# Performance work log

Hardware: AMD Instinct MI355X
Metric: run time of the kernel (lower is better)

Reference implementation:

```python
import jax, jax.numpy as jnp
import numpy as np

# E2M1 FP4 value table: codes 0-7 positive, 8-15 negative (sign bit = MSB)
FP4_LUT = jnp.array([0.0, 0.5, 1.0, 1.5, 2.0, 3.0, 4.0, 6.0,
                     -0.0, -0.5, -1.0, -1.5, -2.0, -3.0, -4.0, -6.0],
                    dtype=jnp.float32)
GROUP = 32  # MX microscaling block size


def _dequant(codes, scales):
    # codes: [O, I] int in [0,16); scales: [O, I//GROUP] power-of-two floats
    vals = FP4_LUT[codes]                          # [O, I]
    return vals * jnp.repeat(scales, GROUP, axis=1)  # broadcast group scale


def setup_inputs() -> dict:
    key = jax.random.key(0)
    ks = jax.random.split(key, 7)
    T, D, G = 8192, 4096, GROUP
    x = jax.random.normal(ks[0], (T, D), dtype=jnp.float32)
    w1_codes = jax.random.randint(ks[1], (D, D), 0, 16, dtype=jnp.int32)
    w1_scales = (2.0 ** jax.random.randint(ks[2], (D, D // G), -6, 2)).astype(jnp.float32)
    b1 = jax.random.normal(ks[3], (D,), dtype=jnp.float32) * 0.01
    w2_codes = jax.random.randint(ks[4], (D, D), 0, 16, dtype=jnp.int32)
    w2_scales = (2.0 ** jax.random.randint(ks[5], (D, D // G), -6, 2)).astype(jnp.float32)
    b2 = jax.random.normal(ks[6], (D,), dtype=jnp.float32) * 0.01
    return {"x": x, "w1_codes": w1_codes, "w1_scales": w1_scales, "b1": b1,
            "w2_codes": w2_codes, "w2_scales": w2_scales, "b2": b2}


def reference(x, w1_codes, w1_scales, b1, w2_codes, w2_scales, b2):
    # first MXFP4 quant linear: y = x @ dequant(W1)^T + b1
    h = x @ _dequant(w1_codes, w1_scales).T + b1
    # second MXFP4 quant linear
    y = h @ _dequant(w2_codes, w2_scales).T + b2
    return y
```

## Files before the change

### kernel.cpp

```cpp
#include <hip/hip_runtime.h>


typedef __bf16 bf16;
typedef bf16 bf16x8 __attribute__((ext_vector_type(8)));
typedef float f32x4 __attribute__((ext_vector_type(4)));
typedef int intx4 __attribute__((ext_vector_type(4)));

#define T_DIM 8192
#define D_DIM 4096

__device__ __forceinline__ void gld_lds16(const void* g, void* l) {
    __builtin_amdgcn_global_load_lds(
        (const __attribute__((address_space(1))) void*)g,
        (__attribute__((address_space(3))) void*)l,
        16, 0, 0);
}

__global__ __launch_bounds__(256) void dequant_kernel(
    const int* __restrict__ codes, const float* __restrict__ scales,
    bf16* __restrict__ out)
{
    const size_t tid = (size_t)blockIdx.x * 256 + threadIdx.x;
    const size_t e = tid * 8;
    const int row = (int)(e >> 12);
    const int col = (int)(e & 4095);
    const float s = scales[(size_t)row * (D_DIM / 32) + (col >> 5)];
    const intx4 c0 = *(const intx4*)(codes + e);
    const intx4 c1 = *(const intx4*)(codes + e + 4);
    bf16x8 o;
#pragma unroll
    for (int i = 0; i < 8; ++i) {
        const int c = (i < 4) ? c0[i] : c1[i - 4];
        float v = (float)((0xC8643210u >> ((c & 7) * 4)) & 0xF) * 0.5f;
        v = (c & 8) ? -v : v;
        o[i] = (bf16)(v * s);
    }
    *(bf16x8*)(out + e) = o;
}

__global__ __launch_bounds__(256) void f32_to_bf16_kernel(
    const float* __restrict__ in, bf16* __restrict__ out)
{
    const size_t tid = (size_t)blockIdx.x * 256 + threadIdx.x;
    const size_t e = tid * 8;
    const float4 a = *(const float4*)(in + e);
    const float4 b = *(const float4*)(in + e + 4);
    bf16x8 o;
    o[0] = (bf16)a.x; o[1] = (bf16)a.y; o[2] = (bf16)a.z; o[3] = (bf16)a.w;
    o[4] = (bf16)b.x; o[5] = (bf16)b.y; o[6] = (bf16)b.z; o[7] = (bf16)b.w;
    *(bf16x8*)(out + e) = o;
}

__device__ __forceinline__ bf16x8 fragr(const char* slot, int row, int qbs) {
    return *(const bf16x8*)(slot + row * 64 + qbs);
}

template <bool OUT_BF16>
__global__ __launch_bounds__(512, 2) void gemm_bt_8ph(
    const bf16* __restrict__ A, const bf16* __restrict__ B,
    const float* __restrict__ bias, void* __restrict__ Cout,
    int M, int N, int K)
{
    __shared__ alignas(128) char lds[131072];
    char* ldsA = lds;
    char* ldsB = lds + 65536;

    const int u = threadIdx.x;
    const int lane = u & 63;
    const int wave = u >> 6;
    const int wm = wave >> 2;
    const int wn = wave & 3;
    const int fr = lane & 15;
    const int qbs = ((lane >> 4) * 16) ^ ((fr & 6) << 3);

    const int nwg = gridDim.x * gridDim.y;
    const int bid0 = blockIdx.y * gridDim.x + blockIdx.x;
    const int cpx = nwg >> 3;
    const int sbid = (bid0 & 7) * cpx + (bid0 >> 3);
    const int m0 = (sbid / gridDim.x) * 256;
    const int n0 = (sbid % gridDim.x) * 256;

    const int r0 = u >> 2;
    const int cb = ((u & 3) * 16) ^ ((r0 & 6) << 3);
    const bf16* pa = A + (size_t)(m0 + r0) * K + (cb >> 1);
    const bf16* pb = B + (size_t)(n0 + r0) * K + (cb >> 1);
    const size_t rstep = (size_t)128 * K;

#define STAGE_A(SLOT, KB) do {                                                 \
    gld_lds16(pa + (KB),         ldsA + (SLOT) * 16384 + u * 16);              \
    gld_lds16(pa + rstep + (KB), ldsA + (SLOT) * 16384 + 8192 + u * 16);       \
  } while (0)
#define STAGE_B(SLOT, KB) do {                                                 \
    gld_lds16(pb + (KB),         ldsB + (SLOT) * 16384 + u * 16);              \
    gld_lds16(pb + rstep + (KB), ldsB + (SLOT) * 16384 + 8192 + u * 16);       \
  } while (0)
#define AS(s) (ldsA + (s) * 16384)
#define BS(s) (ldsB + (s) * 16384)

    const int arow0 = wm * 128 + fr;
    const int brow0 = wn * 64 + fr;

    f32x4 acc[8][4] = {};
    bf16x8 aq[4], bq[4];

#define PHASE(ASLOT, BSLOT, MH, READB, STAGE_STMT, DO_VM)                      \
  do {                                                                         \
    if (READB) {                                                               \
      bq[0] = fragr(BSLOT, brow0,      qbs);                                   \
      bq[1] = fragr(BSLOT, brow0 + 16, qbs);                                   \
      bq[2] = fragr(BSLOT, brow0 + 32, qbs);                                   \
      bq[3] = fragr(BSLOT, brow0 + 48, qbs);                                   \
    }                                                                          \
    aq[0] = fragr(ASLOT, arow0 + (MH) * 64,      qbs);                         \
    aq[1] = fragr(ASLOT, arow0 + (MH) * 64 + 16, qbs);                         \
    aq[2] = fragr(ASLOT, arow0 + (MH) * 64 + 32, qbs);                         \
    aq[3] = fragr(ASLOT, arow0 + (MH) * 64 + 48, qbs);                         \
    STAGE_STMT;                                                                \
    __builtin_amdgcn_s_barrier();                                              \
    asm volatile("s_waitcnt lgkmcnt(0)" ::: "memory");                         \
    __builtin_amdgcn_s_setprio(1);                                             \
    _Pragma("unroll")                                                          \
    for (int jj = 0; jj < 4; ++jj) {                                           \
      _Pragma("unroll")                                                        \
      for (int ii = 0; ii < 4; ++ii)                                           \
        acc[(MH) * 4 + ii][jj] = __builtin_amdgcn_mfma_f32_16x16x32_bf16(      \
            aq[ii], bq[jj], acc[(MH) * 4 + ii][jj], 0, 0, 0);                  \
    }                                                                          \
    __builtin_amdgcn_s_setprio(0);                                             \
    if (DO_VM) { asm volatile("s_waitcnt vmcnt(6)" ::: "memory"); }            \
    __builtin_amdgcn_s_barrier();                                              \
  } while (0)

    STAGE_A(0, 0);
    STAGE_B(0, 0);
    STAGE_A(1, 32);
    STAGE_B(1, 32);
    STAGE_A(2, 64);
    STAGE_B(2, 64);
    STAGE_B(3, 96);
    asm volatile("s_waitcnt vmcnt(6)" ::: "memory");
    __builtin_amdgcn_s_barrier();

    const int NT = K >> 6;
    const int NI = NT >> 1;

    for (int it = 0; it < NI; ++it) {
        const int t = it * 2;
        const int k1 = (t + 1) * 64;
        const int k2 = ((t + 2) < NT ? (t + 2) : (NT - 1)) * 64;
        const int k3 = ((t + 3) < NT ? (t + 3) : (NT - 1)) * 64;
        PHASE(AS(0), BS(0), 0, 1, STAGE_A(3, k1 + 32), 0);
        PHASE(AS(0), BS(0), 1, 0, STAGE_B(0, k2),      0);
        PHASE(AS(1), BS(1), 0, 1, STAGE_A(0, k2),      0);
        PHASE(AS(1), BS(1), 1, 0, STAGE_B(1, k2 + 32), 1);
        PHASE(AS(2), BS(2), 0, 1, STAGE_A(1, k2 + 32), 0);
        PHASE(AS(2), BS(2), 1, 0, STAGE_B(2, k3),      0);
        PHASE(AS(3), BS(3), 0, 1, STAGE_A(2, k3),      0);
        PHASE(AS(3), BS(3), 1, 0, STAGE_B(3, k3 + 32), 1);
    }

#undef PHASE
#undef STAGE_A
#undef STAGE_B
#undef AS
#undef BS

    const int cn = fr;
    const int q4 = (lane >> 4) * 4;
#pragma unroll
    for (int j = 0; j < 4; ++j) {
        const int gn = n0 + wn * 64 + j * 16 + cn;
        const float bv = bias[gn];
#pragma unroll
        for (int mf = 0; mf < 8; ++mf) {
            const int gm = m0 + wm * 128 + mf * 16 + q4;
#pragma unroll
            for (int r = 0; r < 4; ++r) {
                const float v = acc[mf][j][r] + bv;
                const size_t idx = (size_t)(gm + r) * N + gn;
                if (OUT_BF16) ((bf16*)Cout)[idx] = (bf16)v;
                else          ((float*)Cout)[idx] = v;
            }
        }
    }
    (void)M;
}

extern "C" void kernel_launch(void* const* d_in, const int* in_sizes, int n_in,
                              void* d_out, int out_size, void* d_ws, size_t ws_size,
                              hipStream_t stream)
{
    const float* x         = (const float*)d_in[0];
    const int*   w1_codes  = (const int*)d_in[1];
    const float* w1_scales = (const float*)d_in[2];
    const float* b1        = (const float*)d_in[3];
    const int*   w2_codes  = (const int*)d_in[4];
    const float* w2_scales = (const float*)d_in[5];
    const float* b2        = (const float*)d_in[6];
    float* y = (float*)d_out;

    char* ws = (char*)d_ws;
    bf16* Xb = (bf16*)ws;
    bf16* Hb = (bf16*)(ws + (size_t)T_DIM * D_DIM * 2);
    bf16* Wd = (bf16*)(ws + (size_t)2 * T_DIM * D_DIM * 2);

    f32_to_bf16_kernel<<<(T_DIM * (size_t)D_DIM) / 8 / 256, 256, 0, stream>>>(x, Xb);
    dequant_kernel<<<(D_DIM * (size_t)D_DIM) / 8 / 256, 256, 0, stream>>>(w1_codes, w1_scales, Wd);
    dim3 grid(D_DIM / 256, T_DIM / 256);
    gemm_bt_8ph<true><<<grid, 512, 0, stream>>>(Xb, Wd, b1, (void*)Hb,
                                                T_DIM, D_DIM, D_DIM);
    dequant_kernel<<<(D_DIM * (size_t)D_DIM) / 8 / 256, 256, 0, stream>>>(w2_codes, w2_scales, Wd);
    gemm_bt_8ph<false><<<grid, 512, 0, stream>>>(Hb, Wd, b2, (void*)y,
                                                 T_DIM, D_DIM, D_DIM);
}
```

Before: 755.7 us.

## Double-buffer LDS fragment reads in registers to overlap with MFMA

Result: no change. 768.7 us (+1.7%).

```diff
diff --git a/kernel.cpp b/kernel.cpp
--- a/kernel.cpp
+++ b/kernel.cpp
@@ -81,9 +81,9 @@
     const int n0 = (sbid % gridDim.x) * 256;
 
     const int r0 = u >> 2;
-    const int cb = ((u & 3) * 16) ^ ((r0 & 6) << 3);
-    const bf16* pa = A + (size_t)(m0 + r0) * K + (cb >> 1);
-    const bf16* pb = B + (size_t)(n0 + r0) * K + (cb >> 1);
+    const int cbs = ((u & 3) * 16) ^ ((r0 & 6) << 3);
+    const bf16* pa = A + (size_t)(m0 + r0) * K + (cbs >> 1);
+    const bf16* pb = B + (size_t)(n0 + r0) * K + (cbs >> 1);
     const size_t rstep = (size_t)128 * K;
 
 #define STAGE_A(SLOT, KB) do {                                                 \
@@ -101,30 +101,33 @@
     const int brow0 = wn * 64 + fr;
 
     f32x4 acc[8][4] = {};
-    bf16x8 aq[4], bq[4];
-
-#define PHASE(ASLOT, BSLOT, MH, READB, STAGE_STMT, DO_VM)                      \
+    bf16x8 aq0[4], aq1[4], bq0[4], bq1[4];
+
+#define READ_A(DST, ASLOT, MH) do {                                            \
+    DST[0] = fragr((ASLOT), arow0 + (MH) * 64,      qbs);                      \
+    DST[1] = fragr((ASLOT), arow0 + (MH) * 64 + 16, qbs);                      \
+    DST[2] = fragr((ASLOT), arow0 + (MH) * 64 + 32, qbs);                      \
+    DST[3] = fragr((ASLOT), arow0 + (MH) * 64 + 48, qbs);                      \
+  } while (0)
+#define READ_B(DST, BSLOT) do {                                                \
+    DST[0] = fragr((BSLOT), brow0,      qbs);                                  \
+    DST[1] = fragr((BSLOT), brow0 + 16, qbs);                                  \
+    DST[2] = fragr((BSLOT), brow0 + 32, qbs);                                  \
+    DST[3] = fragr((BSLOT), brow0 + 48, qbs);                                  \
+  } while (0)
+
+#define PHASE(PF_STMT, STAGE_STMT, AQ, BQ, MH, DO_VM)                          \
   do {                                                                         \
-    if (READB) {                                                               \
-      bq[0] = fragr(BSLOT, brow0,      qbs);                                   \
-      bq[1] = fragr(BSLOT, brow0 + 16, qbs);                                   \
-      bq[2] = fragr(BSLOT, brow0 + 32, qbs);                                   \
-      bq[3] = fragr(BSLOT, brow0 + 48, qbs);                                   \
-    }                                                                          \
-    aq[0] = fragr(ASLOT, arow0 + (MH) * 64,      qbs);                         \
-    aq[1] = fragr(ASLOT, arow0 + (MH) * 64 + 16, qbs);                         \
-    aq[2] = fragr(ASLOT, arow0 + (MH) * 64 + 32, qbs);                         \
-    aq[3] = fragr(ASLOT, arow0 + (MH) * 64 + 48, qbs);                         \
+    PF_STMT;                                                                   \
     STAGE_STMT;                                                                \
     __builtin_amdgcn_s_barrier();                                              \
-    asm volatile("s_waitcnt lgkmcnt(0)" ::: "memory");                         \
     __builtin_amdgcn_s_setprio(1);                                             \
     _Pragma("unroll")                                                          \
     for (int jj = 0; jj < 4; ++jj) {                                           \
       _Pragma("unroll")                                                        \
       for (int ii = 0; ii < 4; ++ii)                                           \
         acc[(MH) * 4 + ii][jj] = __builtin_amdgcn_mfma_f32_16x16x32_bf16(      \
-            aq[ii], bq[jj], acc[(MH) * 4 + ii][jj], 0, 0, 0);                  \
+            AQ[ii], BQ[jj], acc[(MH) * 4 + ii][jj], 0, 0, 0);                  \
     }                                                                          \
     __builtin_amdgcn_s_setprio(0);                                             \
     if (DO_VM) { asm volatile("s_waitcnt vmcnt(6)" ::: "memory"); }            \
@@ -141,6 +144,9 @@
     asm volatile("s_waitcnt vmcnt(6)" ::: "memory");
     __builtin_amdgcn_s_barrier();
 
+    READ_A(aq0, AS(0), 0);
+    READ_B(bq0, BS(0));
+
     const int NT = K >> 6;
     const int NI = NT >> 1;
 
@@ -149,17 +155,27 @@
         const int k1 = (t + 1) * 64;
         const int k2 = ((t + 2) < NT ? (t + 2) : (NT - 1)) * 64;
         const int k3 = ((t + 3) < NT ? (t + 3) : (NT - 1)) * 64;
-        PHASE(AS(0), BS(0), 0, 1, STAGE_A(3, k1 + 32), 0);
-        PHASE(AS(0), BS(0), 1, 0, STAGE_B(0, k2),      0);
-        PHASE(AS(1), BS(1), 0, 1, STAGE_A(0, k2),      0);
-        PHASE(AS(1), BS(1), 1, 0, STAGE_B(1, k2 + 32), 1);
-        PHASE(AS(2), BS(2), 0, 1, STAGE_A(1, k2 + 32), 0);
-        PHASE(AS(2), BS(2), 1, 0, STAGE_B(2, k3),      0);
-        PHASE(AS(3), BS(3), 0, 1, STAGE_A(2, k3),      0);
-        PHASE(AS(3), BS(3), 1, 0, STAGE_B(3, k3 + 32), 1);
+        PHASE(READ_A(aq1, AS(0), 1),
+              STAGE_A(3, k1 + 32), aq0, bq0, 0, 0);
+        PHASE(READ_A(aq0, AS(1), 0); READ_B(bq1, BS(1)),
+              STAGE_B(0, k2),      aq1, bq0, 1, 1);
+        PHASE(READ_A(aq1, AS(1), 1),
+              STAGE_A(0, k2),      aq0, bq1, 0, 0);
+        PHASE(READ_A(aq0, AS(2), 0); READ_B(bq0, BS(2)),
+              STAGE_B(1, k2 + 32), aq1, bq1, 1, 1);
+        PHASE(READ_A(aq1, AS(2), 1),
+              STAGE_A(1, k2 + 32), aq0, bq0, 0, 0);
+        PHASE(READ_A(aq0, AS(3), 0); READ_B(bq1, BS(3)),
+              STAGE_B(2, k3),      aq1, bq0, 1, 1);
+        PHASE(READ_A(aq1, AS(3), 1),
+              STAGE_A(2, k3),      aq0, bq1, 0, 0);
+        PHASE(READ_A(aq0, AS(0), 0); READ_B(bq0, BS(0)),
+              STAGE_B(3, k3 + 32), aq1, bq1, 1, 1);
     }
 
 #undef PHASE
+#undef READ_A
+#undef READ_B
 #undef STAGE_A
 #undef STAGE_B
 #undef AS
```
